# Kernel tuning notes

Measured on AMD Instinct MI355X. Metric: run time of the kernel, lower is better.

Reference implementation:

```python
import jax, jax.numpy as jnp
import numpy as np

IN_FEAT = 3 * 32 * 32  # channels*height*width
HID = 1024
CLASSES = 10
EPS = 1e-5


def binarize(w):
    # Deterministic BinaryConnect: sign(w) in {-1, +1} (sign(0) -> +1)
    return jnp.where(w >= 0, 1.0, -1.0).astype(w.dtype)


def batchnorm(h, gamma, beta):
    # training-mode BatchNorm1d: biased batch stats over batch axis
    mean = jnp.mean(h, axis=0)
    var = jnp.var(h, axis=0)
    return gamma * (h - mean) * jax.lax.rsqrt(var + EPS) + beta


def setup_inputs() -> dict:
    key = jax.random.key(0)
    ks = jax.random.split(key, 6)
    x = jax.random.normal(ks[0], (8192, 3, 32, 32), dtype=jnp.float32)
    # latent real-valued weights, torch Linear layout [out, in], kaiming-ish scale
    W1 = jax.random.normal(ks[1], (HID, IN_FEAT), dtype=jnp.float32) * (1.0 / np.sqrt(IN_FEAT))
    W2 = jax.random.normal(ks[2], (HID, HID), dtype=jnp.float32) * (1.0 / np.sqrt(HID))
    W3 = jax.random.normal(ks[3], (HID, HID), dtype=jnp.float32) * (1.0 / np.sqrt(HID))
    W4 = jax.random.normal(ks[4], (CLASSES, HID), dtype=jnp.float32) * (1.0 / np.sqrt(HID))
    g1 = jnp.ones((HID,), jnp.float32); b1 = jnp.zeros((HID,), jnp.float32)
    g2 = jnp.ones((HID,), jnp.float32); b2 = jnp.zeros((HID,), jnp.float32)
    g3 = jnp.ones((HID,), jnp.float32); b3 = jnp.zeros((HID,), jnp.float32)
    return {"x": x, "W1": W1, "W2": W2, "W3": W3, "W4": W4,
            "g1": g1, "b1": b1, "g2": g2, "b2": b2, "g3": g3, "b3": b3}


def reference(x, W1, W2, W3, W4, g1, b1, g2, b2, g3, b3):
    h = x.reshape(-1, IN_FEAT)                       # [B, 3072]
    h = jax.nn.relu(h @ binarize(W1).T)              # [B, 1024]
    h = batchnorm(h, g1, b1)
    h = jax.nn.relu(h @ binarize(W2).T)
    h = batchnorm(h, g2, b2)
    h = jax.nn.relu(h @ binarize(W3).T)
    h = batchnorm(h, g3, b3)
    return h @ binarize(W4).T                        # [B, classes]
```

## Files before the change

kernel.cpp:

```cpp
#include <hip/hip_runtime.h>
#include <stdint.h>

typedef unsigned short u16;
typedef __attribute__((ext_vector_type(8))) unsigned short ushort8;
typedef __attribute__((ext_vector_type(4))) unsigned short ushort4v;
typedef __attribute__((ext_vector_type(8))) __bf16 bf16x8;
typedef __attribute__((ext_vector_type(4))) float f32x4;

__device__ __forceinline__ u16 f2bf(float f) {
    union { float f; unsigned int u; } v; v.f = f;
    unsigned int r = v.u + 0x7FFFu + ((v.u >> 16) & 1u);
    return (u16)(r >> 16);
}
__device__ __forceinline__ float bf2f(u16 b) {
    union { unsigned int u; float f; } v; v.u = ((unsigned int)b) << 16;
    return v.f;
}

typedef __attribute__((address_space(1))) const uint32_t* gptr_t;
typedef __attribute__((address_space(3))) uint32_t* lptr_t;
__device__ __forceinline__ void async_copy16(const void* g, void* l) {
    __builtin_amdgcn_global_load_lds((gptr_t)g, (lptr_t)l, 16, 0, 0);
}


__global__ __launch_bounds__(256) void f32_to_bf16_kernel(
    const float* __restrict__ in, u16* __restrict__ out, int n8)
{
    int i = blockIdx.x * 256 + threadIdx.x;
    if (i >= n8) return;
    const float4* p = (const float4*)(in + (size_t)i * 8);
    float4 x0 = p[0], x1 = p[1];
    ushort8 o;
    o[0] = f2bf(x0.x); o[1] = f2bf(x0.y); o[2] = f2bf(x0.z); o[3] = f2bf(x0.w);
    o[4] = f2bf(x1.x); o[5] = f2bf(x1.y); o[6] = f2bf(x1.z); o[7] = f2bf(x1.w);
    *(ushort8*)(out + (size_t)i * 8) = o;
}

__global__ __launch_bounds__(256) void binarize_kernel(
    const float* __restrict__ in, u16* __restrict__ out, int n8)
{
    int i = blockIdx.x * 256 + threadIdx.x;
    if (i >= n8) return;
    const float4* p = (const float4*)(in + (size_t)i * 8);
    float4 x0 = p[0], x1 = p[1];
    ushort8 o;
    o[0] = x0.x >= 0.f ? 0x3F80 : 0xBF80;
    o[1] = x0.y >= 0.f ? 0x3F80 : 0xBF80;
    o[2] = x0.z >= 0.f ? 0x3F80 : 0xBF80;
    o[3] = x0.w >= 0.f ? 0x3F80 : 0xBF80;
    o[4] = x1.x >= 0.f ? 0x3F80 : 0xBF80;
    o[5] = x1.y >= 0.f ? 0x3F80 : 0xBF80;
    o[6] = x1.z >= 0.f ? 0x3F80 : 0xBF80;
    o[7] = x1.w >= 0.f ? 0x3F80 : 0xBF80;
    *(ushort8*)(out + (size_t)i * 8) = o;
}

__global__ __launch_bounds__(256) void build_w4t(
    const float* __restrict__ W4, u16* __restrict__ W4T)
{
    int idx = blockIdx.x * 256 + threadIdx.x;
    int k = idx >> 4, c = idx & 15;
    u16 v = 0;
    if (c < 10) v = (W4[(size_t)c * 1024 + k] >= 0.f) ? 0x3F80 : 0xBF80;
    W4T[idx] = v;
}

__global__ __launch_bounds__(256) void rescale_w(
    const float* __restrict__ W, const float* __restrict__ ss,
    u16* __restrict__ Wp, float* __restrict__ bias)
{
    const int lane = threadIdx.x & 63;
    const int wid  = threadIdx.x >> 6;
    const int r    = blockIdx.x * 4 + wid;
    float bsum = 0.f;
    #pragma unroll
    for (int k0 = 0; k0 < 1024; k0 += 256) {
        int k = k0 + lane * 4;
        float4 w  = *(const float4*)(W + (size_t)r * 1024 + k);
        float4 sc = *(const float4*)(ss + k);
        float4 sh = *(const float4*)(ss + 1024 + k);
        ushort4v o;
        o[0] = f2bf(w.x >= 0.f ? sc.x : -sc.x);
        o[1] = f2bf(w.y >= 0.f ? sc.y : -sc.y);
        o[2] = f2bf(w.z >= 0.f ? sc.z : -sc.z);
        o[3] = f2bf(w.w >= 0.f ? sc.w : -sc.w);
        bsum += (w.x >= 0.f ? sh.x : -sh.x) + (w.y >= 0.f ? sh.y : -sh.y)
              + (w.z >= 0.f ? sh.z : -sh.z) + (w.w >= 0.f ? sh.w : -sh.w);
        *(ushort4v*)(Wp + (size_t)r * 1024 + k) = o;
    }
    #pragma unroll
    for (int off = 32; off; off >>= 1) bsum += __shfl_xor(bsum, off, 64);
    if (lane == 0) bias[r] = bsum;
}

__device__ __forceinline__ void xcd_map(int& mm, int& jj) {
    const int d = blockIdx.x + blockIdx.y * gridDim.x;
    mm = (d & 7) + (d >> 6) * 8;
    jj = (d >> 3) & 7;
}


__global__ __launch_bounds__(256) void gemm_fused(
    const u16* __restrict__ A, const u16* __restrict__ B,
    u16* __restrict__ H, const float* __restrict__ bias,
    float* __restrict__ partS, float* __restrict__ partS2,
    int M, int N, int K)
{
    __shared__ __align__(16) u16 As[2][128 * 64];
    __shared__ __align__(16) u16 Bs[2][128 * 64];

    const int tid  = threadIdx.x;
    const int wid  = tid >> 6;
    const int lane = tid & 63;
    const int lr   = lane & 15;
    const int hk   = lane >> 4;
    const int x7   = lr & 7;
    const int wr   = wid >> 1;
    const int wc   = wid & 1;

    int mm, jj;
    xcd_map(mm, jj);
    const int row0 = mm * 128;
    const int col0 = jj * 128;

    const int s_r = tid >> 3;
    const int s_c = (((tid & 7) ^ (s_r & 7)) << 3);
    const u16* gA = A + (size_t)(row0 + s_r) * K + s_c;
    const u16* gB = B + (size_t)(col0 + s_r) * K + s_c;

    int a_base[4], b_base[4];
    #pragma unroll
    for (int i = 0; i < 4; ++i) a_base[i] = (wr * 64 + i * 16 + lr) * 64;
    #pragma unroll
    for (int j = 0; j < 4; ++j) b_base[j] = (wc * 64 + j * 16 + lr) * 64;
    const int xs0 = ((hk)     ^ x7) << 3;
    const int xs1 = ((hk + 4) ^ x7) << 3;

    f32x4 acc[4][4];
    #pragma unroll
    for (int i = 0; i < 4; ++i)
        #pragma unroll
        for (int j = 0; j < 4; ++j)
            acc[i][j] = (f32x4){0.f, 0.f, 0.f, 0.f};

    const int NT = K >> 6;

    auto STAGE = [&](int buf, int t) {
        const u16* pa = gA + (size_t)t * 64;
        const u16* pb = gB + (size_t)t * 64;
        #pragma unroll
        for (int i = 0; i < 4; ++i)
            async_copy16(pa + (size_t)i * 32 * K, &As[buf][i * 2048 + wid * 512]);
        #pragma unroll
        for (int i = 0; i < 4; ++i)
            async_copy16(pb + (size_t)i * 32 * K, &Bs[buf][i * 2048 + wid * 512]);
    };

    STAGE(0, 0);
    STAGE(1, 1);

    for (int t = 0; t < NT; ++t) {
        const int buf = t & 1;
        if (t + 1 < NT) asm volatile("s_waitcnt vmcnt(8)" ::: "memory");
        else            asm volatile("s_waitcnt vmcnt(0)" ::: "memory");
        __builtin_amdgcn_s_barrier();

        bf16x8 af[4][2], bg[4][2];
        #pragma unroll
        for (int i = 0; i < 4; ++i) {
            af[i][0] = *(const bf16x8*)&As[buf][a_base[i] + xs0];
            af[i][1] = *(const bf16x8*)&As[buf][a_base[i] + xs1];
        }
        #pragma unroll
        for (int j = 0; j < 4; ++j) {
            bg[j][0] = *(const bf16x8*)&Bs[buf][b_base[j] + xs0];
            bg[j][1] = *(const bf16x8*)&Bs[buf][b_base[j] + xs1];
        }
        asm volatile("s_waitcnt lgkmcnt(0)" ::: "memory");
        __builtin_amdgcn_sched_barrier(0);
        __builtin_amdgcn_s_barrier();

        if (t + 2 < NT) STAGE(buf, t + 2);

        __builtin_amdgcn_s_setprio(1);
        #pragma unroll
        for (int kk = 0; kk < 2; ++kk)
            #pragma unroll
            for (int i = 0; i < 4; ++i)
                #pragma unroll
                for (int j = 0; j < 4; ++j)
                    acc[i][j] = __builtin_amdgcn_mfma_f32_16x16x32_bf16(
                        af[i][kk], bg[j][kk], acc[i][j], 0, 0, 0);
        __builtin_amdgcn_s_setprio(0);
    }

    const int er = hk * 4;
    #pragma unroll
    for (int j = 0; j < 4; ++j) {
        const int c = col0 + wc * 64 + j * 16 + lr;
        const float bj = bias ? bias[c] : 0.f;
        float s = 0.f, s2 = 0.f;
        #pragma unroll
        for (int i = 0; i < 4; ++i) {
            const int r = row0 + wr * 64 + i * 16 + er;
            #pragma unroll
            for (int b2 = 0; b2 < 4; ++b2) {
                float x = acc[i][j][b2] + bj;
                x = x > 0.f ? x : 0.f;
                s += x; s2 += x * x;
                H[(size_t)(r + b2) * N + c] = f2bf(x);
            }
        }
        s  += __shfl_xor(s, 16, 64);  s  += __shfl_xor(s, 32, 64);
        s2 += __shfl_xor(s2, 16, 64); s2 += __shfl_xor(s2, 32, 64);
        if (hk == 0) {
            const int p = mm * 2 + wr;
            partS [(size_t)p * 1024 + c] = s;
            partS2[(size_t)p * 1024 + c] = s2;
        }
    }
}


__global__ __launch_bounds__(256) void bn_finalize(
    const float* __restrict__ partS, const float* __restrict__ partS2,
    const float* __restrict__ gamma, const float* __restrict__ beta,
    float* __restrict__ ss)
{
    int c = blockIdx.x * 256 + threadIdx.x;
    float s = 0.f, s2 = 0.f;
    for (int i = 0; i < 128; ++i) {
        s  += partS [(size_t)i * 1024 + c];
        s2 += partS2[(size_t)i * 1024 + c];
    }
    float mean = s * (1.0f / 8192.0f);
    float var  = fmaxf(s2 * (1.0f / 8192.0f) - mean * mean, 0.f);
    float sc   = gamma[c] * rsqrtf(var + 1e-5f);
    ss[c]        = sc;
    ss[1024 + c] = beta[c] - mean * sc;
}


__global__ __launch_bounds__(256) void head_kernel(
    const u16* __restrict__ H, const u16* __restrict__ W4T,
    const float* __restrict__ ss, float* __restrict__ out)
{
    const int lane = threadIdx.x & 63;
    const int wid  = threadIdx.x >> 6;
    const int r    = blockIdx.x * 4 + wid;

    float acc[10];
    #pragma unroll
    for (int c = 0; c < 10; c++) acc[c] = 0.f;

    #pragma unroll
    for (int j = 0; j < 16; ++j) {
        int k = j * 64 + lane;
        float a = fmaf(bf2f(H[(size_t)r * 1024 + k]), ss[k], ss[1024 + k]);
        ushort8 w0 = *(const ushort8*)(W4T + (size_t)k * 16);
        acc[0] += a * bf2f(w0[0]); acc[1] += a * bf2f(w0[1]);
        acc[2] += a * bf2f(w0[2]); acc[3] += a * bf2f(w0[3]);
        acc[4] += a * bf2f(w0[4]); acc[5] += a * bf2f(w0[5]);
        acc[6] += a * bf2f(w0[6]); acc[7] += a * bf2f(w0[7]);
        u16 w8 = W4T[(size_t)k * 16 + 8];
        u16 w9 = W4T[(size_t)k * 16 + 9];
        acc[8] += a * bf2f(w8);    acc[9] += a * bf2f(w9);
    }
    #pragma unroll
    for (int c = 0; c < 10; c++) {
        float s = acc[c];
        #pragma unroll
        for (int off = 32; off > 0; off >>= 1) s += __shfl_xor(s, off, 64);
        acc[c] = s;
    }
    if (lane == 0) {
        #pragma unroll
        for (int c = 0; c < 10; c++) out[(size_t)r * 10 + c] = acc[c];
    }
}


extern "C" void kernel_launch(void* const* d_in, const int* in_sizes, int n_in,
                              void* d_out, int out_size, void* d_ws, size_t ws_size,
                              hipStream_t stream) {
    const float* x  = (const float*)d_in[0];
    const float* W1 = (const float*)d_in[1];
    const float* W2 = (const float*)d_in[2];
    const float* W3 = (const float*)d_in[3];
    const float* W4 = (const float*)d_in[4];
    const float* g1 = (const float*)d_in[5];
    const float* b1 = (const float*)d_in[6];
    const float* g2 = (const float*)d_in[7];
    const float* b2 = (const float*)d_in[8];
    const float* g3 = (const float*)d_in[9];
    const float* b3 = (const float*)d_in[10];
    float* out = (float*)d_out;

    char* ws = (char*)d_ws;
    u16*   Xb     = (u16*)  (ws + 0);
    u16*   Hb0    = (u16*)  (ws + 50331648);
    u16*   Hb1    = (u16*)  (ws + 67108864);
    u16*   W1b    = (u16*)  (ws + 83886080);
    u16*   W2p    = (u16*)  (ws + 90177536);
    u16*   W3p    = (u16*)  (ws + 92274688);
    u16*   W4T    = (u16*)  (ws + 94371840);
    float* partS  = (float*)(ws + 94404608);
    float* partS2 = (float*)(ws + 94928896);
    float* ss     = (float*)(ws + 95453184);
    float* bias2  = (float*)(ws + 95461376);
    float* bias3  = (float*)(ws + 95465472);

    f32_to_bf16_kernel<<<12288, 256, 0, stream>>>(x, Xb, 3145728);
    binarize_kernel<<<1536, 256, 0, stream>>>(W1, W1b, 393216);
    build_w4t<<<64, 256, 0, stream>>>(W4, W4T);

    dim3 gemm_grid(64, 8);

    gemm_fused<<<gemm_grid, 256, 0, stream>>>(Xb, W1b, Hb0, nullptr, partS, partS2, 8192, 1024, 3072);
    bn_finalize<<<4, 256, 0, stream>>>(partS, partS2, g1, b1, ss);
    rescale_w<<<256, 256, 0, stream>>>(W2, ss, W2p, bias2);

    gemm_fused<<<gemm_grid, 256, 0, stream>>>(Hb0, W2p, Hb1, bias2, partS, partS2, 8192, 1024, 1024);
    bn_finalize<<<4, 256, 0, stream>>>(partS, partS2, g2, b2, ss);
    rescale_w<<<256, 256, 0, stream>>>(W3, ss, W3p, bias3);

    gemm_fused<<<gemm_grid, 256, 0, stream>>>(Hb1, W3p, Hb0, bias3, partS, partS2, 8192, 1024, 1024);
    bn_finalize<<<4, 256, 0, stream>>>(partS, partS2, g3, b3, ss);

    head_kernel<<<2048, 256, 0, stream>>>(Hb0, W4T, ss, out);
}
```

Before: 190.3 us.

## Switch GEMM to 32x32x16 MFMA, overlap LDS reads with MFMA, merge prep kernels

The fused GEMM now uses 32x32x16 bf16 MFMA on 2x2 accumulator tiles per wave instead of 16x16x32 on 4x4 tiles, and the epilogue row mapping and stat reduction are rewritten to match. LDS fragment loads are issued per k-slice with partial lgkmcnt waits, so the first MFMAs start before all fragments arrive and the rest run after the next stage's async copies are issued. The three preprocessing kernels are merged into one launch with block-range dispatch. The aim is fewer MFMA and LDS instructions and less launch overhead, at the cost of a more complex fragment swizzle and row mapping that could be wrong.

New measurement: 197.2 us. 1.04x slower.

```diff
diff --git a/kernel.cpp b/kernel.cpp
--- a/kernel.cpp
+++ b/kernel.cpp
@@ -6,6 +6,7 @@
 typedef __attribute__((ext_vector_type(4))) unsigned short ushort4v;
 typedef __attribute__((ext_vector_type(8))) __bf16 bf16x8;
 typedef __attribute__((ext_vector_type(4))) float f32x4;
+typedef __attribute__((ext_vector_type(16))) float f32x16;
 
 __device__ __forceinline__ u16 f2bf(float f) {
     union { float f; unsigned int u; } v; v.f = f;
@@ -24,46 +25,41 @@
 }
 
 
-__global__ __launch_bounds__(256) void f32_to_bf16_kernel(
-    const float* __restrict__ in, u16* __restrict__ out, int n8)
-{
-    int i = blockIdx.x * 256 + threadIdx.x;
-    if (i >= n8) return;
-    const float4* p = (const float4*)(in + (size_t)i * 8);
-    float4 x0 = p[0], x1 = p[1];
-    ushort8 o;
-    o[0] = f2bf(x0.x); o[1] = f2bf(x0.y); o[2] = f2bf(x0.z); o[3] = f2bf(x0.w);
-    o[4] = f2bf(x1.x); o[5] = f2bf(x1.y); o[6] = f2bf(x1.z); o[7] = f2bf(x1.w);
-    *(ushort8*)(out + (size_t)i * 8) = o;
-}
-
-__global__ __launch_bounds__(256) void binarize_kernel(
-    const float* __restrict__ in, u16* __restrict__ out, int n8)
-{
-    int i = blockIdx.x * 256 + threadIdx.x;
-    if (i >= n8) return;
-    const float4* p = (const float4*)(in + (size_t)i * 8);
-    float4 x0 = p[0], x1 = p[1];
-    ushort8 o;
-    o[0] = x0.x >= 0.f ? 0x3F80 : 0xBF80;
-    o[1] = x0.y >= 0.f ? 0x3F80 : 0xBF80;
-    o[2] = x0.z >= 0.f ? 0x3F80 : 0xBF80;
-    o[3] = x0.w >= 0.f ? 0x3F80 : 0xBF80;
-    o[4] = x1.x >= 0.f ? 0x3F80 : 0xBF80;
-    o[5] = x1.y >= 0.f ? 0x3F80 : 0xBF80;
-    o[6] = x1.z >= 0.f ? 0x3F80 : 0xBF80;
-    o[7] = x1.w >= 0.f ? 0x3F80 : 0xBF80;
-    *(ushort8*)(out + (size_t)i * 8) = o;
-}
-
-__global__ __launch_bounds__(256) void build_w4t(
-    const float* __restrict__ W4, u16* __restrict__ W4T)
-{
-    int idx = blockIdx.x * 256 + threadIdx.x;
-    int k = idx >> 4, c = idx & 15;
-    u16 v = 0;
-    if (c < 10) v = (W4[(size_t)c * 1024 + k] >= 0.f) ? 0x3F80 : 0xBF80;
-    W4T[idx] = v;
+__global__ __launch_bounds__(256) void pre_kernel(
+    const float* __restrict__ x, const float* __restrict__ W1,
+    const float* __restrict__ W4,
+    u16* __restrict__ Xb, u16* __restrict__ W1b, u16* __restrict__ W4T)
+{
+    const int b = blockIdx.x;
+    if (b < 12288) {
+        int i = b * 256 + threadIdx.x;
+        const float4* p = (const float4*)(x + (size_t)i * 8);
+        float4 x0 = p[0], x1 = p[1];
+        ushort8 o;
+        o[0] = f2bf(x0.x); o[1] = f2bf(x0.y); o[2] = f2bf(x0.z); o[3] = f2bf(x0.w);
+        o[4] = f2bf(x1.x); o[5] = f2bf(x1.y); o[6] = f2bf(x1.z); o[7] = f2bf(x1.w);
+        *(ushort8*)(Xb + (size_t)i * 8) = o;
+    } else if (b < 13824) {
+        int i = (b - 12288) * 256 + threadIdx.x;
+        const float4* p = (const float4*)(W1 + (size_t)i * 8);
+        float4 x0 = p[0], x1 = p[1];
+        ushort8 o;
+        o[0] = x0.x >= 0.f ? 0x3F80 : 0xBF80;
+        o[1] = x0.y >= 0.f ? 0x3F80 : 0xBF80;
+        o[2] = x0.z >= 0.f ? 0x3F80 : 0xBF80;
+        o[3] = x0.w >= 0.f ? 0x3F80 : 0xBF80;
+        o[4] = x1.x >= 0.f ? 0x3F80 : 0xBF80;
+        o[5] = x1.y >= 0.f ? 0x3F80 : 0xBF80;
+        o[6] = x1.z >= 0.f ? 0x3F80 : 0xBF80;
+        o[7] = x1.w >= 0.f ? 0x3F80 : 0xBF80;
+        *(ushort8*)(W1b + (size_t)i * 8) = o;
+    } else {
+        int idx = (b - 13824) * 256 + threadIdx.x;
+        int k = idx >> 4, c = idx & 15;
+        u16 v = 0;
+        if (c < 10) v = (W4[(size_t)c * 1024 + k] >= 0.f) ? 0x3F80 : 0xBF80;
+        W4T[idx] = v;
+    }
 }
 
 __global__ __launch_bounds__(256) void rescale_w(
@@ -113,9 +109,9 @@
     const int tid  = threadIdx.x;
     const int wid  = tid >> 6;
     const int lane = tid & 63;
-    const int lr   = lane & 15;
-    const int hk   = lane >> 4;
-    const int x7   = lr & 7;
+    const int cl   = lane & 31;
+    const int hi   = lane >> 5;
+    const int x7r  = cl & 7;
     const int wr   = wid >> 1;
     const int wc   = wid & 1;
 
@@ -129,20 +125,19 @@
     const u16* gA = A + (size_t)(row0 + s_r) * K + s_c;
     const u16* gB = B + (size_t)(col0 + s_r) * K + s_c;
 
-    int a_base[4], b_base[4];
-    #pragma unroll
-    for (int i = 0; i < 4; ++i) a_base[i] = (wr * 64 + i * 16 + lr) * 64;
-    #pragma unroll
-    for (int j = 0; j < 4; ++j) b_base[j] = (wc * 64 + j * 16 + lr) * 64;
-    const int xs0 = ((hk)     ^ x7) << 3;
-    const int xs1 = ((hk + 4) ^ x7) << 3;
-
-    f32x4 acc[4][4];
-    #pragma unroll
-    for (int i = 0; i < 4; ++i)
-        #pragma unroll
-        for (int j = 0; j < 4; ++j)
-            acc[i][j] = (f32x4){0.f, 0.f, 0.f, 0.f};
+    const int a_base0 = (wr * 64 +  0 + cl) * 64;
+    const int a_base1 = (wr * 64 + 32 + cl) * 64;
+    const int b_base0 = (wc * 64 +  0 + cl) * 64;
+    const int b_base1 = (wc * 64 + 32 + cl) * 64;
+
+    f32x16 acc[2][2];
+    #pragma unroll
+    for (int i = 0; i < 2; ++i)
+        #pragma unroll
+        for (int j = 0; j < 2; ++j)
+            #pragma unroll
+            for (int r = 0; r < 16; ++r)
+                acc[i][j][r] = 0.f;
 
     const int NT = K >> 6;
 
@@ -166,17 +161,32 @@
         else            asm volatile("s_waitcnt vmcnt(0)" ::: "memory");
         __builtin_amdgcn_s_barrier();
 
-        bf16x8 af[4][2], bg[4][2];
-        #pragma unroll
-        for (int i = 0; i < 4; ++i) {
-            af[i][0] = *(const bf16x8*)&As[buf][a_base[i] + xs0];
-            af[i][1] = *(const bf16x8*)&As[buf][a_base[i] + xs1];
+        bf16x8 af0[4], af1[4], bg0[4], bg1[4];
+        #pragma unroll
+        for (int kt = 0; kt < 4; ++kt) {
+            const int xk = ((((kt << 1) | hi) ^ x7r) << 3);
+            af0[kt] = *(const bf16x8*)&As[buf][a_base0 + xk];
+            af1[kt] = *(const bf16x8*)&As[buf][a_base1 + xk];
+            bg0[kt] = *(const bf16x8*)&Bs[buf][b_base0 + xk];
+            bg1[kt] = *(const bf16x8*)&Bs[buf][b_base1 + xk];
+            __builtin_amdgcn_sched_barrier(0);
         }
-        #pragma unroll
-        for (int j = 0; j < 4; ++j) {
-            bg[j][0] = *(const bf16x8*)&Bs[buf][b_base[j] + xs0];
-            bg[j][1] = *(const bf16x8*)&Bs[buf][b_base[j] + xs1];
-        }
+
+        asm volatile("s_waitcnt lgkmcnt(12)" ::: "memory");
+        __builtin_amdgcn_sched_barrier(0);
+        __builtin_amdgcn_s_setprio(1);
+        acc[0][0] = __builtin_amdgcn_mfma_f32_32x32x16_bf16(af0[0], bg0[0], acc[0][0], 0, 0, 0);
+        acc[0][1] = __builtin_amdgcn_mfma_f32_32x32x16_bf16(af0[0], bg1[0], acc[0][1], 0, 0, 0);
+        acc[1][0] = __builtin_amdgcn_mfma_f32_32x32x16_bf16(af1[0], bg0[0], acc[1][0], 0, 0, 0);
+        acc[1][1] = __builtin_amdgcn_mfma_f32_32x32x16_bf16(af1[0], bg1[0], acc[1][1], 0, 0, 0);
+        asm volatile("s_waitcnt lgkmcnt(8)" ::: "memory");
+        __builtin_amdgcn_sched_barrier(0);
+        acc[0][0] = __builtin_amdgcn_mfma_f32_32x32x16_bf16(af0[1], bg0[1], acc[0][0], 0, 0, 0);
+        acc[0][1] = __builtin_amdgcn_mfma_f32_32x32x16_bf16(af0[1], bg1[1], acc[0][1], 0, 0, 0);
+        acc[1][0] = __builtin_amdgcn_mfma_f32_32x32x16_bf16(af1[1], bg0[1], acc[1][0], 0, 0, 0);
+        acc[1][1] = __builtin_amdgcn_mfma_f32_32x32x16_bf16(af1[1], bg1[1], acc[1][1], 0, 0, 0);
+        __builtin_amdgcn_s_setprio(0);
+
         asm volatile("s_waitcnt lgkmcnt(0)" ::: "memory");
         __builtin_amdgcn_sched_barrier(0);
         __builtin_amdgcn_s_barrier();
@@ -184,37 +194,37 @@
         if (t + 2 < NT) STAGE(buf, t + 2);
 
         __builtin_amdgcn_s_setprio(1);
-        #pragma unroll
-        for (int kk = 0; kk < 2; ++kk)
-            #pragma unroll
-            for (int i = 0; i < 4; ++i)
-                #pragma unroll
-                for (int j = 0; j < 4; ++j)
-                    acc[i][j] = __builtin_amdgcn_mfma_f32_16x16x32_bf16(
-                        af[i][kk], bg[j][kk], acc[i][j], 0, 0, 0);
+        acc[0][0] = __builtin_amdgcn_mfma_f32_32x32x16_bf16(af0[2], bg0[2], acc[0][0], 0, 0, 0);
+        acc[0][1] = __builtin_amdgcn_mfma_f32_32x32x16_bf16(af0[2], bg1[2], acc[0][1], 0, 0, 0);
+        acc[1][0] = __builtin_amdgcn_mfma_f32_32x32x16_bf16(af1[2], bg0[2], acc[1][0], 0, 0, 0);
+        acc[1][1] = __builtin_amdgcn_mfma_f32_32x32x16_bf16(af1[2], bg1[2], acc[1][1], 0, 0, 0);
+        acc[0][0] = __builtin_amdgcn_mfma_f32_32x32x16_bf16(af0[3], bg0[3], acc[0][0], 0, 0, 0);
+        acc[0][1] = __builtin_amdgcn_mfma_f32_32x32x16_bf16(af0[3], bg1[3], acc[0][1], 0, 0, 0);
+        acc[1][0] = __builtin_amdgcn_mfma_f32_32x32x16_bf16(af1[3], bg0[3], acc[1][0], 0, 0, 0);
+        acc[1][1] = __builtin_amdgcn_mfma_f32_32x32x16_bf16(af1[3], bg1[3], acc[1][1], 0, 0, 0);
         __builtin_amdgcn_s_setprio(0);
     }
 
-    const int er = hk * 4;
-    #pragma unroll
-    for (int j = 0; j < 4; ++j) {
-        const int c = col0 + wc * 64 + j * 16 + lr;
+    #pragma unroll
+    for (int j = 0; j < 2; ++j) {
+        const int c = col0 + wc * 64 + j * 32 + cl;
         const float bj = bias ? bias[c] : 0.f;
         float s = 0.f, s2 = 0.f;
         #pragma unroll
-        for (int i = 0; i < 4; ++i) {
-            const int r = row0 + wr * 64 + i * 16 + er;
+        for (int i = 0; i < 2; ++i) {
             #pragma unroll
-            for (int b2 = 0; b2 < 4; ++b2) {
-                float x = acc[i][j][b2] + bj;
+            for (int reg = 0; reg < 16; ++reg) {
+                const int rl = (reg & 3) + 8 * (reg >> 2) + 4 * hi;
+                const int r = row0 + wr * 64 + i * 32 + rl;
+                float x = acc[i][j][reg] + bj;
                 x = x > 0.f ? x : 0.f;
                 s += x; s2 += x * x;
-                H[(size_t)(r + b2) * N + c] = f2bf(x);
+                H[(size_t)r * N + c] = f2bf(x);
             }
         }
-        s  += __shfl_xor(s, 16, 64);  s  += __shfl_xor(s, 32, 64);
-        s2 += __shfl_xor(s2, 16, 64); s2 += __shfl_xor(s2, 32, 64);
-        if (hk == 0) {
+        s  += __shfl_xor(s, 32, 64);
+        s2 += __shfl_xor(s2, 32, 64);
+        if (hi == 0) {
             const int p = mm * 2 + wr;
             partS [(size_t)p * 1024 + c] = s;
             partS2[(size_t)p * 1024 + c] = s2;
@@ -311,9 +321,7 @@
     float* bias2  = (float*)(ws + 95461376);
     float* bias3  = (float*)(ws + 95465472);
 
-    f32_to_bf16_kernel<<<12288, 256, 0, stream>>>(x, Xb, 3145728);
-    binarize_kernel<<<1536, 256, 0, stream>>>(W1, W1b, 393216);
-    build_w4t<<<64, 256, 0, stream>>>(W4, W4T);
+    pre_kernel<<<13888, 256, 0, stream>>>(x, W1, W4, Xb, W1b, W4T);
 
     dim3 gemm_grid(64, 8);
 
```
